# Optimization experiments

Hardware: AMD Instinct MI355X
Metric: run time of the kernel (lower is better)

The kernel has to match this reference:

```python
import jax, jax.numpy as jnp
import numpy as np

K = 2            # top-k experts
TEMP = 1.0       # temperature
LN_EPS = 1e-5

def setup_inputs() -> dict:
    key = jax.random.key(0)
    B, S, D, E = 4, 4096, 2048, 64
    k0, k1, k2, k3 = jax.random.split(key, 4)
    x = jax.random.normal(k0, (B, S, D), dtype=jnp.float32)
    Wg = jax.random.normal(k1, (E, D), dtype=jnp.float32) * 0.02       # base_gate weight [out,in]
    gamma = jnp.ones((D,), jnp.float32)                                 # LayerNorm weight
    beta = jnp.zeros((D,), jnp.float32)                                 # LayerNorm bias
    W1 = jax.random.normal(k2, (D // 2, D), dtype=jnp.float32) * 0.02   # diff_pred linear1
    W2 = jax.random.normal(k3, (1, D // 2), dtype=jnp.float32) * 0.02   # diff_pred linear2
    return {"x": x, "Wg": Wg, "gamma": gamma, "beta": beta, "W1": W1, "W2": W2}

def reference(x, Wg, gamma, beta, W1, W2):
    # base expert logits: [B,S,E]
    logits = jnp.einsum('bsd,ed->bse', x, Wg)
    # difficulty predictor: LN -> Linear -> GELU -> Linear -> sigmoid, [B,S,1]
    mu = jnp.mean(x, axis=-1, keepdims=True)
    var = jnp.var(x, axis=-1, keepdims=True)
    h = (x - mu) * jax.lax.rsqrt(var + LN_EPS) * gamma + beta
    h1 = jax.nn.gelu(jnp.einsum('bsd,hd->bsh', h, W1), approximate=False)
    diff = jax.nn.sigmoid(jnp.einsum('bsh,oh->bso', h1, W2))
    # modulate + temperature (eval mode: no jitter / mask_drop)
    logits = logits / (1.0 + diff) * (1.0 / TEMP)
    probs_soft = jax.nn.softmax(logits, axis=-1)
    # top-k selection
    _, idx = jax.lax.top_k(logits, K)                    # [B,S,K]
    hard_any = jnp.max(jax.nn.one_hot(idx, logits.shape[-1], dtype=probs_soft.dtype), axis=2)  # [B,S,E]
    probs_st = hard_any - probs_soft + probs_soft        # faithful to source (no detach)
    scores = jnp.take_along_axis(probs_st, idx, axis=-1)  # [B,S,K]
    scores = scores / jnp.maximum(jnp.sum(scores, axis=-1, keepdims=True), 1e-9)
    importance = jax.lax.stop_gradient(jnp.mean(probs_soft, axis=(0, 1)))  # [E]
    load = jax.lax.stop_gradient(jnp.mean(hard_any, axis=(0, 1)))          # [E]
    return (idx, scores, probs_soft, importance, load)
```

## Files before the change

kernel.cpp:

```cpp
#include <hip/hip_runtime.h>
#include <math.h>

#define BS_TOK 16384
#define DIM    2048
#define NEXP   64
#define DHID   1024
#define GKS    4
#define KSL    (DIM / GKS)

typedef __attribute__((ext_vector_type(8))) _Float16 f16x8;
typedef __attribute__((ext_vector_type(4))) float    f32x4;

#define GLOBAL_AS const __attribute__((address_space(1))) void*
#define LDS_AS    __attribute__((address_space(3))) void*

__device__ __forceinline__ float gelu_f(float x) {
  return 0.5f * x * (1.0f + erff(x * 0.70710678118654752440f));
}

__global__ __launch_bounds__(256) void ln_kernel(const float* __restrict__ X,
                                                 const float* __restrict__ gamma,
                                                 const float* __restrict__ beta,
                                                 _Float16* __restrict__ H) {
  const int tid  = threadIdx.x;
  const int w    = tid >> 6, lane = tid & 63;
  const int t    = blockIdx.x * 4 + w;
  const float* xr = X + (size_t)t * DIM;
  float4 xv[8];
#pragma unroll
  for (int j = 0; j < 4; ++j) {
    const int c0 = (j * 64 + lane) * 8;
    xv[j * 2]     = *(const float4*)(xr + c0);
    xv[j * 2 + 1] = *(const float4*)(xr + c0 + 4);
  }
  float s = 0.f, q = 0.f;
#pragma unroll
  for (int j = 0; j < 8; ++j) {
    s += (xv[j].x + xv[j].y) + (xv[j].z + xv[j].w);
    q += (xv[j].x * xv[j].x + xv[j].y * xv[j].y) + (xv[j].z * xv[j].z + xv[j].w * xv[j].w);
  }
#pragma unroll
  for (int off = 32; off > 0; off >>= 1) {
    s += __shfl_xor(s, off);
    q += __shfl_xor(q, off);
  }
  const float mu  = s * (1.0f / DIM);
  const float var = q * (1.0f / DIM) - mu * mu;
  const float rs  = rsqrtf(var + 1e-5f);
#pragma unroll
  for (int j = 0; j < 4; ++j) {
    const int c0 = (j * 64 + lane) * 8;
    const float4 g0 = *(const float4*)(gamma + c0);
    const float4 g1 = *(const float4*)(gamma + c0 + 4);
    const float4 b0 = *(const float4*)(beta + c0);
    const float4 b1 = *(const float4*)(beta + c0 + 4);
    const float4 a = xv[j * 2], b = xv[j * 2 + 1];
    f16x8 h;
    h[0] = (_Float16)((a.x - mu) * rs * g0.x + b0.x);
    h[1] = (_Float16)((a.y - mu) * rs * g0.y + b0.y);
    h[2] = (_Float16)((a.z - mu) * rs * g0.z + b0.z);
    h[3] = (_Float16)((a.w - mu) * rs * g0.w + b0.w);
    h[4] = (_Float16)((b.x - mu) * rs * g1.x + b1.x);
    h[5] = (_Float16)((b.y - mu) * rs * g1.y + b1.y);
    h[6] = (_Float16)((b.z - mu) * rs * g1.z + b1.z);
    h[7] = (_Float16)((b.w - mu) * rs * g1.w + b1.w);
    *(f16x8*)(H + (size_t)t * DIM + c0) = h;
  }
}

__global__ __launch_bounds__(256) void w1cast_kernel(const float* __restrict__ W1,
                                                     _Float16* __restrict__ W1h) {
  const int i = (blockIdx.x * 256 + threadIdx.x) * 8;
  const float4 a = *(const float4*)(W1 + i);
  const float4 b = *(const float4*)(W1 + i + 4);
  f16x8 o;
  o[0] = (_Float16)a.x; o[1] = (_Float16)a.y; o[2] = (_Float16)a.z; o[3] = (_Float16)a.w;
  o[4] = (_Float16)b.x; o[5] = (_Float16)b.y; o[6] = (_Float16)b.z; o[7] = (_Float16)b.w;
  *(f16x8*)(W1h + i) = o;
}

__global__ __launch_bounds__(256) void gate_kernel(const float* __restrict__ X,
                                                   const float* __restrict__ Wg,
                                                   float* __restrict__ logitsP) {
  __shared__ float sX[16][68];
  __shared__ float sW[16][68];
  const int tid  = threadIdx.x;
  const int m0   = blockIdx.x * 64;
  const int k0   = blockIdx.y * KSL;
  const int srow = tid >> 2;
  const int skq  = tid & 3;
  const int ty   = tid >> 4;
  const int tx   = tid & 15;
  const float* xb = X  + (size_t)(m0 + srow) * DIM + k0 + skq * 4;
  const float* wb = Wg + (size_t)srow * DIM + k0 + skq * 4;
  float acc[4][4] = {};
  float4 rx = *(const float4*)xb;
  float4 rw = *(const float4*)wb;
  for (int kt = 0; kt < KSL; kt += 16) {
    __syncthreads();
    sX[skq * 4 + 0][srow] = rx.x;
    sX[skq * 4 + 1][srow] = rx.y;
    sX[skq * 4 + 2][srow] = rx.z;
    sX[skq * 4 + 3][srow] = rx.w;
    sW[skq * 4 + 0][srow] = rw.x;
    sW[skq * 4 + 1][srow] = rw.y;
    sW[skq * 4 + 2][srow] = rw.z;
    sW[skq * 4 + 3][srow] = rw.w;
    const int ktn = (kt + 16 < KSL) ? kt + 16 : 0;
    rx = *(const float4*)(xb + ktn);
    rw = *(const float4*)(wb + ktn);
    __syncthreads();
#pragma unroll
    for (int k = 0; k < 16; ++k) {
      const float4 a4 = *(const float4*)&sX[k][ty * 4];
      const float4 b4 = *(const float4*)&sW[k][tx * 4];
      const float av[4] = {a4.x, a4.y, a4.z, a4.w};
      const float bv[4] = {b4.x, b4.y, b4.z, b4.w};
#pragma unroll
      for (int i = 0; i < 4; ++i)
#pragma unroll
        for (int j = 0; j < 4; ++j) acc[i][j] += av[i] * bv[j];
    }
  }
  float* op = logitsP + (size_t)blockIdx.y * (BS_TOK * NEXP)
            + (size_t)(m0 + ty * 4) * NEXP + tx * 4;
#pragma unroll
  for (int i = 0; i < 4; ++i) {
    float4 o;
    o.x = acc[i][0]; o.y = acc[i][1]; o.z = acc[i][2]; o.w = acc[i][3];
    *(float4*)(op + (size_t)i * NEXP) = o;
  }
}

__global__ __launch_bounds__(256) void g2_kernel(const _Float16* __restrict__ H,
                                                 const _Float16* __restrict__ W1h,
                                                 const float* __restrict__ W2,
                                                 float* __restrict__ diffz) {
  __shared__ __align__(16) _Float16 sA[128 * 32];
  __shared__ __align__(16) _Float16 sB[128 * 32];
  const int bid = blockIdx.x;
  const int c   = bid & 7;
  const int j   = bid >> 3;
  const int m0  = (c * 16 + (j >> 3)) * 128;
  const int n0  = (j & 7) * 128;
  const int tid  = threadIdx.x;
  const int w    = tid >> 6, lane = tid & 63;
  const int wr   = w >> 1,  wc   = w & 1;
  const int col  = lane & 15, quad = lane >> 4;
  const int row0 = tid >> 2,  kp = tid & 3;
  const int row1 = row0 + 64;
  const _Float16* gA0 = H   + (size_t)(m0 + row0) * DIM + kp * 8;
  const _Float16* gA1 = H   + (size_t)(m0 + row1) * DIM + kp * 8;
  const _Float16* gB0 = W1h + (size_t)(n0 + row0) * DIM + kp * 8;
  const _Float16* gB1 = W1h + (size_t)(n0 + row1) * DIM + kp * 8;
  f32x4 acc[4][4] = {};
  for (int kt = 0; kt < DIM; kt += 32) {
    __syncthreads();
    __builtin_amdgcn_global_load_lds((GLOBAL_AS)(gA0 + kt), (LDS_AS)(sA + tid * 8), 16, 0, 0);
    __builtin_amdgcn_global_load_lds((GLOBAL_AS)(gA1 + kt), (LDS_AS)(sA + (256 + tid) * 8), 16, 0, 0);
    __builtin_amdgcn_global_load_lds((GLOBAL_AS)(gB0 + kt), (LDS_AS)(sB + tid * 8), 16, 0, 0);
    __builtin_amdgcn_global_load_lds((GLOBAL_AS)(gB1 + kt), (LDS_AS)(sB + (256 + tid) * 8), 16, 0, 0);
    __syncthreads();
    f16x8 af[4], bf[4];
#pragma unroll
    for (int mi = 0; mi < 4; ++mi)
      af[mi] = *(const f16x8*)(sA + (wr * 64 + mi * 16 + col) * 32 + quad * 8);
#pragma unroll
    for (int ni = 0; ni < 4; ++ni)
      bf[ni] = *(const f16x8*)(sB + (wc * 64 + ni * 16 + col) * 32 + quad * 8);
#pragma unroll
    for (int mi = 0; mi < 4; ++mi)
#pragma unroll
      for (int ni = 0; ni < 4; ++ni)
        acc[mi][ni] = __builtin_amdgcn_mfma_f32_16x16x32_f16(af[mi], bf[ni], acc[mi][ni], 0, 0, 0);
  }
  float w2v[4];
#pragma unroll
  for (int ni = 0; ni < 4; ++ni) w2v[ni] = W2[n0 + wc * 64 + ni * 16 + col];
#pragma unroll
  for (int mi = 0; mi < 4; ++mi) {
#pragma unroll
    for (int reg = 0; reg < 4; ++reg) {
      float v = 0.f;
#pragma unroll
      for (int ni = 0; ni < 4; ++ni) v += gelu_f(acc[mi][ni][reg]) * w2v[ni];
      v += __shfl_xor(v, 1);
      v += __shfl_xor(v, 2);
      v += __shfl_xor(v, 4);
      v += __shfl_xor(v, 8);
      if (col == 0)
        atomicAdd(diffz + m0 + wr * 64 + mi * 16 + quad * 4 + reg, v);
    }
  }
}

__global__ __launch_bounds__(256) void finalize_kernel(const float* __restrict__ logitsP,
                                                       const float* __restrict__ diffz,
                                                       float* __restrict__ out_idx,
                                                       float* __restrict__ out_scores,
                                                       float* __restrict__ out_probs,
                                                       float* __restrict__ imp_acc,
                                                       float* __restrict__ load_acc) {
  const int tid  = threadIdx.x;
  const int w    = tid >> 6, lane = tid & 63;
  const size_t PS = (size_t)BS_TOK * NEXP;
  float acc_imp = 0.f, acc_load = 0.f;
  for (int it = 0; it < 8; ++it) {
    const int t    = blockIdx.x * 32 + it * 4 + w;
    const float* lp = logitsP + (size_t)t * NEXP + lane;
    const float L  = ((lp[0] + lp[PS]) + lp[2 * PS]) + lp[3 * PS];
    const float z  = diffz[t];
    const float d  = 1.0f / (1.0f + expf(-z));
    const float l  = L / (1.0f + d);
    float m = l;
#pragma unroll
    for (int off = 32; off > 0; off >>= 1) m = fmaxf(m, __shfl_xor(m, off));
    float p = expf(l - m);
    float s = p;
#pragma unroll
    for (int off = 32; off > 0; off >>= 1) s += __shfl_xor(s, off);
    p /= s;
    float v = l; int bi = lane;
#pragma unroll
    for (int off = 32; off > 0; off >>= 1) {
      const float ov = __shfl_xor(v, off);
      const int   oi = __shfl_xor(bi, off);
      if (ov > v || (ov == v && oi < bi)) { v = ov; bi = oi; }
    }
    const int i1 = bi;
    float v2 = (lane == i1) ? -INFINITY : l;
    int bi2 = lane;
#pragma unroll
    for (int off = 32; off > 0; off >>= 1) {
      const float ov = __shfl_xor(v2, off);
      const int   oi = __shfl_xor(bi2, off);
      if (ov > v2 || (ov == v2 && oi < bi2)) { v2 = ov; bi2 = oi; }
    }
    const int i2 = bi2;
    const float p1 = __shfl(p, i1);
    const float p2 = __shfl(p, i2);
    const float s1 = (1.0f - p1) + p1;
    const float s2 = (1.0f - p2) + p2;
    const float den = fmaxf(s1 + s2, 1e-9f);
    if (lane == 0) {
      out_idx[t * 2]        = (float)i1;
      out_idx[t * 2 + 1]    = (float)i2;
      out_scores[t * 2]     = s1 / den;
      out_scores[t * 2 + 1] = s2 / den;
    }
    out_probs[(size_t)t * NEXP + lane] = p;
    acc_imp  += p;
    acc_load += (lane == i1 || lane == i2) ? 1.0f : 0.0f;
  }
  __shared__ float s_imp[256];
  __shared__ float s_hard[256];
  s_imp[tid]  = acc_imp;
  s_hard[tid] = acc_load;
  __syncthreads();
  if (tid < 64) {
    const float si = s_imp[tid] + s_imp[64 + tid] + s_imp[128 + tid] + s_imp[192 + tid];
    const float sl = s_hard[tid] + s_hard[64 + tid] + s_hard[128 + tid] + s_hard[192 + tid];
    atomicAdd(imp_acc + tid, si);
    atomicAdd(load_acc + tid, sl);
  }
}

__global__ void scale_kernel(const float* __restrict__ acc,
                             float* __restrict__ out_imp,
                             float* __restrict__ out_load) {
  const int tid = threadIdx.x;
  const float inv = 1.0f / 16384.0f;
  if (tid < 64)       out_imp[tid]        = acc[tid] * inv;
  else if (tid < 128) out_load[tid - 64]  = acc[tid] * inv;
}

extern "C" void kernel_launch(void* const* d_in, const int* in_sizes, int n_in,
                              void* d_out, int out_size, void* d_ws, size_t ws_size,
                              hipStream_t stream) {
  (void)in_sizes; (void)n_in; (void)out_size; (void)ws_size;
  const float* X     = (const float*)d_in[0];
  const float* Wg    = (const float*)d_in[1];
  const float* gamma = (const float*)d_in[2];
  const float* beta  = (const float*)d_in[3];
  const float* W1    = (const float*)d_in[4];
  const float* W2    = (const float*)d_in[5];
  float* out = (float*)d_out;

  char* ws = (char*)d_ws;
  _Float16* H       = (_Float16*)(ws);
  _Float16* W1h     = (_Float16*)(ws + 67108864ull);
  float*    logitsP = (float*)  (ws + 71303168ull);
  float*    diffz   = (float*)  (ws + 88080384ull);
  float*    accs    = (float*)  (ws + 88145920ull);

  float* out_idx    = out;
  float* out_scores = out + 32768;
  float* out_probs  = out + 65536;
  float* out_imp    = out + 1114112;
  float* out_load   = out + 1114176;

  hipMemsetAsync(diffz, 0, 65536ull + 512ull, stream);
  ln_kernel<<<BS_TOK / 4, 256, 0, stream>>>(X, gamma, beta, H);
  w1cast_kernel<<<(DHID * DIM) / (256 * 8), 256, 0, stream>>>(W1, W1h);
  gate_kernel<<<dim3(BS_TOK / 64, GKS), 256, 0, stream>>>(X, Wg, logitsP);
  g2_kernel<<<(DHID / 128) * (BS_TOK / 128), 256, 0, stream>>>(H, W1h, W2, diffz);
  finalize_kernel<<<BS_TOK / 32, 256, 0, stream>>>(logitsP, diffz, out_idx, out_scores,
                                                   out_probs, accs, accs + 64);
  scale_kernel<<<1, 128, 0, stream>>>(accs, out_imp, out_load);
}
```

Baseline: 409.7 us.

## Fuse prep kernels, double-buffer GEMM LDS, merge top-2 reductions, drop scale kernel

Merges the LayerNorm, W1 cast and gate GEMM into one launch that branches on block index, so their memory traffic can overlap and fewer kernels are launched. The g2 GEMM now double-buffers LDS with one barrier per k-step and stores each 16-row fragment contiguously, so the next tile loads while MFMAs run. Finalize computes the max and the top-2 in a single butterfly pass and writes scaled importance and load straight to the output with atomics, which removes the scale kernel. The cost is more LDS per block, possible bank conflicts in the new fragment layout, and an extra memset on the output.

```diff
diff --git a/kernel.cpp b/kernel.cpp
--- a/kernel.cpp
+++ b/kernel.cpp
@@ -13,122 +13,127 @@
 
 #define GLOBAL_AS const __attribute__((address_space(1))) void*
 #define LDS_AS    __attribute__((address_space(3))) void*
+#define GLDS16(g, l) __builtin_amdgcn_global_load_lds((GLOBAL_AS)(g), (LDS_AS)(l), 16, 0, 0)
 
 __device__ __forceinline__ float gelu_f(float x) {
   return 0.5f * x * (1.0f + erff(x * 0.70710678118654752440f));
 }
 
-__global__ __launch_bounds__(256) void ln_kernel(const float* __restrict__ X,
-                                                 const float* __restrict__ gamma,
-                                                 const float* __restrict__ beta,
-                                                 _Float16* __restrict__ H) {
-  const int tid  = threadIdx.x;
-  const int w    = tid >> 6, lane = tid & 63;
-  const int t    = blockIdx.x * 4 + w;
-  const float* xr = X + (size_t)t * DIM;
-  float4 xv[8];
-#pragma unroll
-  for (int j = 0; j < 4; ++j) {
-    const int c0 = (j * 64 + lane) * 8;
-    xv[j * 2]     = *(const float4*)(xr + c0);
-    xv[j * 2 + 1] = *(const float4*)(xr + c0 + 4);
-  }
-  float s = 0.f, q = 0.f;
-#pragma unroll
-  for (int j = 0; j < 8; ++j) {
-    s += (xv[j].x + xv[j].y) + (xv[j].z + xv[j].w);
-    q += (xv[j].x * xv[j].x + xv[j].y * xv[j].y) + (xv[j].z * xv[j].z + xv[j].w * xv[j].w);
-  }
-#pragma unroll
-  for (int off = 32; off > 0; off >>= 1) {
-    s += __shfl_xor(s, off);
-    q += __shfl_xor(q, off);
-  }
-  const float mu  = s * (1.0f / DIM);
-  const float var = q * (1.0f / DIM) - mu * mu;
-  const float rs  = rsqrtf(var + 1e-5f);
-#pragma unroll
-  for (int j = 0; j < 4; ++j) {
-    const int c0 = (j * 64 + lane) * 8;
-    const float4 g0 = *(const float4*)(gamma + c0);
-    const float4 g1 = *(const float4*)(gamma + c0 + 4);
-    const float4 b0 = *(const float4*)(beta + c0);
-    const float4 b1 = *(const float4*)(beta + c0 + 4);
-    const float4 a = xv[j * 2], b = xv[j * 2 + 1];
-    f16x8 h;
-    h[0] = (_Float16)((a.x - mu) * rs * g0.x + b0.x);
-    h[1] = (_Float16)((a.y - mu) * rs * g0.y + b0.y);
-    h[2] = (_Float16)((a.z - mu) * rs * g0.z + b0.z);
-    h[3] = (_Float16)((a.w - mu) * rs * g0.w + b0.w);
-    h[4] = (_Float16)((b.x - mu) * rs * g1.x + b1.x);
-    h[5] = (_Float16)((b.y - mu) * rs * g1.y + b1.y);
-    h[6] = (_Float16)((b.z - mu) * rs * g1.z + b1.z);
-    h[7] = (_Float16)((b.w - mu) * rs * g1.w + b1.w);
-    *(f16x8*)(H + (size_t)t * DIM + c0) = h;
-  }
-}
-
-__global__ __launch_bounds__(256) void w1cast_kernel(const float* __restrict__ W1,
-                                                     _Float16* __restrict__ W1h) {
-  const int i = (blockIdx.x * 256 + threadIdx.x) * 8;
-  const float4 a = *(const float4*)(W1 + i);
-  const float4 b = *(const float4*)(W1 + i + 4);
-  f16x8 o;
-  o[0] = (_Float16)a.x; o[1] = (_Float16)a.y; o[2] = (_Float16)a.z; o[3] = (_Float16)a.w;
-  o[4] = (_Float16)b.x; o[5] = (_Float16)b.y; o[6] = (_Float16)b.z; o[7] = (_Float16)b.w;
-  *(f16x8*)(W1h + i) = o;
-}
-
-__global__ __launch_bounds__(256) void gate_kernel(const float* __restrict__ X,
+#define GATE_NB 1024
+#define LN_NB   4096
+#define CAST_NB 1024
+
+__global__ __launch_bounds__(256) void prep_kernel(const float* __restrict__ X,
                                                    const float* __restrict__ Wg,
+                                                   const float* __restrict__ gamma,
+                                                   const float* __restrict__ beta,
+                                                   const float* __restrict__ W1,
+                                                   _Float16* __restrict__ H,
+                                                   _Float16* __restrict__ W1h,
                                                    float* __restrict__ logitsP) {
+  const int bid = blockIdx.x;
+  const int tid = threadIdx.x;
   __shared__ float sX[16][68];
   __shared__ float sW[16][68];
-  const int tid  = threadIdx.x;
-  const int m0   = blockIdx.x * 64;
-  const int k0   = blockIdx.y * KSL;
-  const int srow = tid >> 2;
-  const int skq  = tid & 3;
-  const int ty   = tid >> 4;
-  const int tx   = tid & 15;
-  const float* xb = X  + (size_t)(m0 + srow) * DIM + k0 + skq * 4;
-  const float* wb = Wg + (size_t)srow * DIM + k0 + skq * 4;
-  float acc[4][4] = {};
-  float4 rx = *(const float4*)xb;
-  float4 rw = *(const float4*)wb;
-  for (int kt = 0; kt < KSL; kt += 16) {
-    __syncthreads();
-    sX[skq * 4 + 0][srow] = rx.x;
-    sX[skq * 4 + 1][srow] = rx.y;
-    sX[skq * 4 + 2][srow] = rx.z;
-    sX[skq * 4 + 3][srow] = rx.w;
-    sW[skq * 4 + 0][srow] = rw.x;
-    sW[skq * 4 + 1][srow] = rw.y;
-    sW[skq * 4 + 2][srow] = rw.z;
-    sW[skq * 4 + 3][srow] = rw.w;
-    const int ktn = (kt + 16 < KSL) ? kt + 16 : 0;
-    rx = *(const float4*)(xb + ktn);
-    rw = *(const float4*)(wb + ktn);
-    __syncthreads();
-#pragma unroll
-    for (int k = 0; k < 16; ++k) {
-      const float4 a4 = *(const float4*)&sX[k][ty * 4];
-      const float4 b4 = *(const float4*)&sW[k][tx * 4];
-      const float av[4] = {a4.x, a4.y, a4.z, a4.w};
-      const float bv[4] = {b4.x, b4.y, b4.z, b4.w};
-#pragma unroll
-      for (int i = 0; i < 4; ++i)
-#pragma unroll
-        for (int j = 0; j < 4; ++j) acc[i][j] += av[i] * bv[j];
-    }
-  }
-  float* op = logitsP + (size_t)blockIdx.y * (BS_TOK * NEXP)
-            + (size_t)(m0 + ty * 4) * NEXP + tx * 4;
-#pragma unroll
-  for (int i = 0; i < 4; ++i) {
-    float4 o;
-    o.x = acc[i][0]; o.y = acc[i][1]; o.z = acc[i][2]; o.w = acc[i][3];
-    *(float4*)(op + (size_t)i * NEXP) = o;
+
+  if (bid < GATE_NB) {
+    const int m0   = (bid >> 2) * 64;
+    const int k0   = (bid & 3) * KSL;
+    const int srow = tid >> 2;
+    const int skq  = tid & 3;
+    const int ty   = tid >> 4;
+    const int tx   = tid & 15;
+    const float* xb = X  + (size_t)(m0 + srow) * DIM + k0 + skq * 4;
+    const float* wb = Wg + (size_t)srow * DIM + k0 + skq * 4;
+    float acc[4][4] = {};
+    float4 rx = *(const float4*)xb;
+    float4 rw = *(const float4*)wb;
+    for (int kt = 0; kt < KSL; kt += 16) {
+      __syncthreads();
+      sX[skq * 4 + 0][srow] = rx.x;
+      sX[skq * 4 + 1][srow] = rx.y;
+      sX[skq * 4 + 2][srow] = rx.z;
+      sX[skq * 4 + 3][srow] = rx.w;
+      sW[skq * 4 + 0][srow] = rw.x;
+      sW[skq * 4 + 1][srow] = rw.y;
+      sW[skq * 4 + 2][srow] = rw.z;
+      sW[skq * 4 + 3][srow] = rw.w;
+      const int ktn = (kt + 16 < KSL) ? kt + 16 : 0;
+      rx = *(const float4*)(xb + ktn);
+      rw = *(const float4*)(wb + ktn);
+      __syncthreads();
+#pragma unroll
+      for (int k = 0; k < 16; ++k) {
+        const float4 a4 = *(const float4*)&sX[k][ty * 4];
+        const float4 b4 = *(const float4*)&sW[k][tx * 4];
+        const float av[4] = {a4.x, a4.y, a4.z, a4.w};
+        const float bv[4] = {b4.x, b4.y, b4.z, b4.w};
+#pragma unroll
+        for (int i = 0; i < 4; ++i)
+#pragma unroll
+          for (int j = 0; j < 4; ++j) acc[i][j] += av[i] * bv[j];
+      }
+    }
+    float* op = logitsP + (size_t)(bid & 3) * (BS_TOK * NEXP)
+              + (size_t)(m0 + ty * 4) * NEXP + tx * 4;
+#pragma unroll
+    for (int i = 0; i < 4; ++i) {
+      float4 o;
+      o.x = acc[i][0]; o.y = acc[i][1]; o.z = acc[i][2]; o.w = acc[i][3];
+      *(float4*)(op + (size_t)i * NEXP) = o;
+    }
+  } else if (bid < GATE_NB + LN_NB) {
+    const int w    = tid >> 6, lane = tid & 63;
+    const int t    = (bid - GATE_NB) * 4 + w;
+    const float* xr = X + (size_t)t * DIM;
+    float4 xv[8];
+#pragma unroll
+    for (int j = 0; j < 4; ++j) {
+      const int c0 = (j * 64 + lane) * 8;
+      xv[j * 2]     = *(const float4*)(xr + c0);
+      xv[j * 2 + 1] = *(const float4*)(xr + c0 + 4);
+    }
+    float s = 0.f, q = 0.f;
+#pragma unroll
+    for (int j = 0; j < 8; ++j) {
+      s += (xv[j].x + xv[j].y) + (xv[j].z + xv[j].w);
+      q += (xv[j].x * xv[j].x + xv[j].y * xv[j].y) + (xv[j].z * xv[j].z + xv[j].w * xv[j].w);
+    }
+#pragma unroll
+    for (int off = 32; off > 0; off >>= 1) {
+      s += __shfl_xor(s, off);
+      q += __shfl_xor(q, off);
+    }
+    const float mu  = s * (1.0f / DIM);
+    const float var = q * (1.0f / DIM) - mu * mu;
+    const float rs  = rsqrtf(var + 1e-5f);
+#pragma unroll
+    for (int j = 0; j < 4; ++j) {
+      const int c0 = (j * 64 + lane) * 8;
+      const float4 g0 = *(const float4*)(gamma + c0);
+      const float4 g1 = *(const float4*)(gamma + c0 + 4);
+      const float4 b0 = *(const float4*)(beta + c0);
+      const float4 b1 = *(const float4*)(beta + c0 + 4);
+      const float4 a = xv[j * 2], b = xv[j * 2 + 1];
+      f16x8 h;
+      h[0] = (_Float16)((a.x - mu) * rs * g0.x + b0.x);
+      h[1] = (_Float16)((a.y - mu) * rs * g0.y + b0.y);
+      h[2] = (_Float16)((a.z - mu) * rs * g0.z + b0.z);
+      h[3] = (_Float16)((a.w - mu) * rs * g0.w + b0.w);
+      h[4] = (_Float16)((b.x - mu) * rs * g1.x + b1.x);
+      h[5] = (_Float16)((b.y - mu) * rs * g1.y + b1.y);
+      h[6] = (_Float16)((b.z - mu) * rs * g1.z + b1.z);
+      h[7] = (_Float16)((b.w - mu) * rs * g1.w + b1.w);
+      *(f16x8*)(H + (size_t)t * DIM + c0) = h;
+    }
+  } else {
+    const int i = ((bid - GATE_NB - LN_NB) * 256 + tid) * 8;
+    const float4 a = *(const float4*)(W1 + i);
+    const float4 b = *(const float4*)(W1 + i + 4);
+    f16x8 o;
+    o[0] = (_Float16)a.x; o[1] = (_Float16)a.y; o[2] = (_Float16)a.z; o[3] = (_Float16)a.w;
+    o[4] = (_Float16)b.x; o[5] = (_Float16)b.y; o[6] = (_Float16)b.z; o[7] = (_Float16)b.w;
+    *(f16x8*)(W1h + i) = o;
   }
 }
 
@@ -136,8 +141,8 @@
                                                  const _Float16* __restrict__ W1h,
                                                  const float* __restrict__ W2,
                                                  float* __restrict__ diffz) {
-  __shared__ __align__(16) _Float16 sA[128 * 32];
-  __shared__ __align__(16) _Float16 sB[128 * 32];
+  __shared__ __align__(16) _Float16 sA[2][4096];
+  __shared__ __align__(16) _Float16 sB[2][4096];
   const int bid = blockIdx.x;
   const int c   = bid & 7;
   const int j   = bid >> 3;
@@ -147,27 +152,36 @@
   const int w    = tid >> 6, lane = tid & 63;
   const int wr   = w >> 1,  wc   = w & 1;
   const int col  = lane & 15, quad = lane >> 4;
-  const int row0 = tid >> 2,  kp = tid & 3;
-  const int row1 = row0 + 64;
-  const _Float16* gA0 = H   + (size_t)(m0 + row0) * DIM + kp * 8;
-  const _Float16* gA1 = H   + (size_t)(m0 + row1) * DIM + kp * 8;
-  const _Float16* gB0 = W1h + (size_t)(n0 + row0) * DIM + kp * 8;
-  const _Float16* gB1 = W1h + (size_t)(n0 + row1) * DIM + kp * 8;
+  const int r    = lane & 15, q = lane >> 4;
+  const int gA   = w * 2;
+  const _Float16* srcA0 = H   + (size_t)(m0 + gA * 16 + r) * DIM + q * 8;
+  const _Float16* srcA1 = srcA0 + (size_t)16 * DIM;
+  const _Float16* srcB0 = W1h + (size_t)(n0 + gA * 16 + r) * DIM + q * 8;
+  const _Float16* srcB1 = srcB0 + (size_t)16 * DIM;
+  const int dOff = gA * 512 + lane * 8;
   f32x4 acc[4][4] = {};
-  for (int kt = 0; kt < DIM; kt += 32) {
+  GLDS16(srcA0, &sA[0][dOff]);
+  GLDS16(srcA1, &sA[0][dOff + 512]);
+  GLDS16(srcB0, &sB[0][dOff]);
+  GLDS16(srcB1, &sB[0][dOff + 512]);
+  for (int it = 0; it < 64; ++it) {
+    const int cb = it & 1;
     __syncthreads();
-    __builtin_amdgcn_global_load_lds((GLOBAL_AS)(gA0 + kt), (LDS_AS)(sA + tid * 8), 16, 0, 0);
-    __builtin_amdgcn_global_load_lds((GLOBAL_AS)(gA1 + kt), (LDS_AS)(sA + (256 + tid) * 8), 16, 0, 0);
-    __builtin_amdgcn_global_load_lds((GLOBAL_AS)(gB0 + kt), (LDS_AS)(sB + tid * 8), 16, 0, 0);
-    __builtin_amdgcn_global_load_lds((GLOBAL_AS)(gB1 + kt), (LDS_AS)(sB + (256 + tid) * 8), 16, 0, 0);
-    __syncthreads();
+    if (it < 63) {
+      const int kt2 = (it + 1) << 5;
+      const int nb  = cb ^ 1;
+      GLDS16(srcA0 + kt2, &sA[nb][dOff]);
+      GLDS16(srcA1 + kt2, &sA[nb][dOff + 512]);
+      GLDS16(srcB0 + kt2, &sB[nb][dOff]);
+      GLDS16(srcB1 + kt2, &sB[nb][dOff + 512]);
+    }
     f16x8 af[4], bf[4];
 #pragma unroll
     for (int mi = 0; mi < 4; ++mi)
-      af[mi] = *(const f16x8*)(sA + (wr * 64 + mi * 16 + col) * 32 + quad * 8);
+      af[mi] = *(const f16x8*)&sA[cb][(wr * 4 + mi) * 512 + lane * 8];
 #pragma unroll
     for (int ni = 0; ni < 4; ++ni)
-      bf[ni] = *(const f16x8*)(sB + (wc * 64 + ni * 16 + col) * 32 + quad * 8);
+      bf[ni] = *(const f16x8*)&sB[cb][(wc * 4 + ni) * 512 + lane * 8];
 #pragma unroll
     for (int mi = 0; mi < 4; ++mi)
 #pragma unroll
@@ -199,8 +213,8 @@
                                                        float* __restrict__ out_idx,
                                                        float* __restrict__ out_scores,
                                                        float* __restrict__ out_probs,
-                                                       float* __restrict__ imp_acc,
-                                                       float* __restrict__ load_acc) {
+                                                       float* __restrict__ out_imp,
+                                                       float* __restrict__ out_load) {
   const int tid  = threadIdx.x;
   const int w    = tid >> 6, lane = tid & 63;
   const size_t PS = (size_t)BS_TOK * NEXP;
@@ -212,31 +226,25 @@
     const float z  = diffz[t];
     const float d  = 1.0f / (1.0f + expf(-z));
     const float l  = L / (1.0f + d);
-    float m = l;
-#pragma unroll
-    for (int off = 32; off > 0; off >>= 1) m = fmaxf(m, __shfl_xor(m, off));
-    float p = expf(l - m);
+    float v1 = l; int i1 = lane;
+    float v2 = -INFINITY; int i2 = 0;
+#pragma unroll
+    for (int off = 32; off > 0; off >>= 1) {
+      const float ov1 = __shfl_xor(v1, off); const int oi1 = __shfl_xor(i1, off);
+      const float ov2 = __shfl_xor(v2, off); const int oi2 = __shfl_xor(i2, off);
+      const bool bwin = (ov1 > v1) || (ov1 == v1 && oi1 < i1);
+      const float w1 = bwin ? ov1 : v1; const int wi1 = bwin ? oi1 : i1;
+      const float l1 = bwin ? v1 : ov1; const int li1 = bwin ? i1 : oi1;
+      const float c2 = bwin ? ov2 : v2; const int ci2 = bwin ? oi2 : i2;
+      const bool s2w = (c2 > l1) || (c2 == l1 && ci2 < li1);
+      v2 = s2w ? c2 : l1; i2 = s2w ? ci2 : li1;
+      v1 = w1; i1 = wi1;
+    }
+    float p = expf(l - v1);
     float s = p;
 #pragma unroll
     for (int off = 32; off > 0; off >>= 1) s += __shfl_xor(s, off);
     p /= s;
-    float v = l; int bi = lane;
-#pragma unroll
-    for (int off = 32; off > 0; off >>= 1) {
-      const float ov = __shfl_xor(v, off);
-      const int   oi = __shfl_xor(bi, off);
-      if (ov > v || (ov == v && oi < bi)) { v = ov; bi = oi; }
-    }
-    const int i1 = bi;
-    float v2 = (lane == i1) ? -INFINITY : l;
-    int bi2 = lane;
-#pragma unroll
-    for (int off = 32; off > 0; off >>= 1) {
-      const float ov = __shfl_xor(v2, off);
-      const int   oi = __shfl_xor(bi2, off);
-      if (ov > v2 || (ov == v2 && oi < bi2)) { v2 = ov; bi2 = oi; }
-    }
-    const int i2 = bi2;
     const float p1 = __shfl(p, i1);
     const float p2 = __shfl(p, i2);
     const float s1 = (1.0f - p1) + p1;
@@ -258,20 +266,12 @@
   s_hard[tid] = acc_load;
   __syncthreads();
   if (tid < 64) {
+    const float inv = 1.0f / (float)BS_TOK;
     const float si = s_imp[tid] + s_imp[64 + tid] + s_imp[128 + tid] + s_imp[192 + tid];
     const float sl = s_hard[tid] + s_hard[64 + tid] + s_hard[128 + tid] + s_hard[192 + tid];
-    atomicAdd(imp_acc + tid, si);
-    atomicAdd(load_acc + tid, sl);
-  }
-}
-
-__global__ void scale_kernel(const float* __restrict__ acc,
-                             float* __restrict__ out_imp,
-                             float* __restrict__ out_load) {
-  const int tid = threadIdx.x;
-  const float inv = 1.0f / 16384.0f;
-  if (tid < 64)       out_imp[tid]        = acc[tid] * inv;
-  else if (tid < 128) out_load[tid - 64]  = acc[tid] * inv;
+    atomicAdd(out_imp + tid, si * inv);
+    atomicAdd(out_load + tid, sl * inv);
+  }
 }
 
 extern "C" void kernel_launch(void* const* d_in, const int* in_sizes, int n_in,
@@ -291,7 +291,6 @@
   _Float16* W1h     = (_Float16*)(ws + 67108864ull);
   float*    logitsP = (float*)  (ws + 71303168ull);
   float*    diffz   = (float*)  (ws + 88080384ull);
-  float*    accs    = (float*)  (ws + 88145920ull);
 
   float* out_idx    = out;
   float* out_scores = out + 32768;
@@ -299,12 +298,11 @@
   float* out_imp    = out + 1114112;
   float* out_load   = out + 1114176;
 
-  hipMemsetAsync(diffz, 0, 65536ull + 512ull, stream);
-  ln_kernel<<<BS_TOK / 4, 256, 0, stream>>>(X, gamma, beta, H);
-  w1cast_kernel<<<(DHID * DIM) / (256 * 8), 256, 0, stream>>>(W1, W1h);
-  gate_kernel<<<dim3(BS_TOK / 64, GKS), 256, 0, stream>>>(X, Wg, logitsP);
+  hipMemsetAsync(diffz, 0, 65536ull, stream);
+  hipMemsetAsync(out_imp, 0, 512ull, stream);
+  prep_kernel<<<GATE_NB + LN_NB + CAST_NB, 256, 0, stream>>>(X, Wg, gamma, beta, W1,
+                                                             H, W1h, logitsP);
   g2_kernel<<<(DHID / 128) * (BS_TOK / 128), 256, 0, stream>>>(H, W1h, W2, diffz);
   finalize_kernel<<<BS_TOK / 32, 256, 0, stream>>>(logitsP, diffz, out_idx, out_scores,
-                                                   out_probs, accs, accs + 64);
-  scale_kernel<<<1, 128, 0, stream>>>(accs, out_imp, out_load);
-}
+                                                   out_probs, out_imp, out_load);
+}
```

After: 445.0 us. 8.6% more time.
